# Kernel tuning notes

Hardware: AMD Instinct MI355X
Metric: run time of the kernel (lower is better)

Reference implementation:

```python
import jax, jax.numpy as jnp
import numpy as np


def setup_inputs() -> dict:
    key = jax.random.key(0)
    B, H, C, T = 8, 8, 64, 2048
    qkv = jax.random.normal(key, (B, 3 * H * C, T), dtype=jnp.float32)
    return {"qkv": qkv, "n_heads": H}


def reference(qkv, n_heads):
    # qkv: (B, 3*H*C, T)
    bs, width, length = qkv.shape
    ch = width // (3 * n_heads)
    q, k, v = jnp.split(qkv, 3, axis=1)          # each (B, H*C, T)
    scale = ch ** (-0.25)
    q = (q * scale).reshape(bs * n_heads, ch, length)
    k = (k * scale).reshape(bs * n_heads, ch, length)
    v = v.reshape(bs * n_heads, ch, length)
    # weight[b, t, s] = sum_c q[b,c,t] * k[b,c,s]
    weight = jnp.einsum('bct,bcs->bts', q, k)
    weight = jax.nn.softmax(weight.astype(jnp.float32), axis=-1).astype(qkv.dtype)
    out = jnp.einsum('bts,bcs->bct', weight, v)   # (B*H, C, T)
    return out.reshape(bs, n_heads * ch, length)
```

## Files before the change

### kernel.cpp

```cpp
#include <hip/hip_runtime.h>

typedef __bf16 bf16x4 __attribute__((ext_vector_type(4)));
typedef __bf16 bf16x8 __attribute__((ext_vector_type(8)));
typedef float floatx4 __attribute__((ext_vector_type(4)));
typedef float floatx16 __attribute__((ext_vector_type(16)));

#define T_SEQ 2048
#define TTILE 256
#define STILE 64
#define LOG2E_SCALE 0.18033688011112042f

__device__ __forceinline__ unsigned pack_bf16(float a, float b) {
    __bf16 x = (__bf16)a, y = (__bf16)b;
    unsigned short ux = __builtin_bit_cast(unsigned short, x);
    unsigned short uy = __builtin_bit_cast(unsigned short, y);
    return (unsigned)ux | ((unsigned)uy << 16);
}

__global__ __launch_bounds__(256, 2) void attn_fused(
    const float* __restrict__ qkv, float* __restrict__ out)
{
    __shared__ __align__(16) __bf16 Kt[STILE][72];
    __shared__ __align__(16) __bf16 Vs[64][72];

    const int tid  = threadIdx.x;
    const int lane = tid & 63;
    const int wave = tid >> 6;
    const int l31  = lane & 31;
    const int g    = lane >> 5;

    const int bh = blockIdx.y;
    const int b = bh >> 3, head = bh & 7;
    const size_t in_base = ((size_t)b * 1536 + head * 64) * T_SEQ;
    const float* Qg = qkv + in_base;
    const float* Kg = qkv + in_base + (size_t)512 * T_SEQ;
    const float* Vg = qkv + in_base + (size_t)1024 * T_SEQ;

    const int tcol0 = blockIdx.x * TTILE + wave * 64 + l31;
    const int tcol1 = tcol0 + 32;

    bf16x8 qf[2][4];
    #pragma unroll
    for (int kb = 0; kb < 4; ++kb)
        #pragma unroll
        for (int j = 0; j < 8; ++j) {
            size_t rowoff = (size_t)(kb * 16 + g * 8 + j) * T_SEQ;
            qf[0][kb][j] = (__bf16)Qg[rowoff + tcol0];
            qf[1][kb][j] = (__bf16)Qg[rowoff + tcol1];
        }

    floatx16 Oa[2][2];
    #pragma unroll
    for (int tt = 0; tt < 2; ++tt)
        #pragma unroll
        for (int mc = 0; mc < 2; ++mc)
            #pragma unroll
            for (int r = 0; r < 16; ++r) Oa[tt][mc][r] = 0.0f;
    float lsum0 = 0.0f, lsum1 = 0.0f;

    int cc[4], ss[4];
    size_t goff[4];
    #pragma unroll
    for (int r = 0; r < 4; ++r) {
        int i = tid + r * 256;
        cc[r] = i >> 4;
        ss[r] = (i & 15) * 4;
        goff[r] = (size_t)cc[r] * T_SEQ + ss[r];
    }
    const int ph = (tid >> 1) & 3;

    floatx4 kr[4], vr[4];
    #pragma unroll
    for (int r = 0; r < 4; ++r) {
        kr[r] = *(const floatx4*)(Kg + goff[r]);
        vr[r] = *(const floatx4*)(Vg + goff[r]);
    }

    for (int s0 = 0; s0 < T_SEQ; s0 += STILE) {
        __syncthreads();
        #pragma unroll
        for (int r = 0; r < 4; ++r) {
            int c = cc[r], s4 = ss[r];
            #pragma unroll
            for (int k = 0; k < 4; ++k) {
                int d = (k + ph) & 3;
                Kt[s4 + d][c] = (__bf16)kr[r][d];
            }
            bf16x4 vb;
            vb[0] = (__bf16)vr[r][0]; vb[1] = (__bf16)vr[r][1];
            vb[2] = (__bf16)vr[r][2]; vb[3] = (__bf16)vr[r][3];
            *(bf16x4*)&Vs[c][s4] = vb;
        }
        __syncthreads();

        if (s0 + STILE < T_SEQ) {
            #pragma unroll
            for (int r = 0; r < 4; ++r) {
                kr[r] = *(const floatx4*)(Kg + goff[r] + s0 + STILE);
                vr[r] = *(const floatx4*)(Vg + goff[r] + s0 + STILE);
            }
        }

        bf16x8 pf[2][4];
        #pragma unroll
        for (int ms = 0; ms < 2; ++ms) {
            floatx16 Sa0, Sa1;
            #pragma unroll
            for (int r = 0; r < 16; ++r) { Sa0[r] = 0.0f; Sa1[r] = 0.0f; }
            #pragma unroll
            for (int kb = 0; kb < 4; ++kb) {
                bf16x8 kf = *(const bf16x8*)&Kt[ms * 32 + l31][kb * 16 + g * 8];
                Sa0 = __builtin_amdgcn_mfma_f32_32x32x16_bf16(kf, qf[0][kb], Sa0, 0, 0, 0);
                Sa1 = __builtin_amdgcn_mfma_f32_32x32x16_bf16(kf, qf[1][kb], Sa1, 0, 0, 0);
            }
            #pragma unroll
            for (int tt = 0; tt < 2; ++tt) {
                const floatx16& Sa = tt ? Sa1 : Sa0;
                float p[16];
                #pragma unroll
                for (int r = 0; r < 16; ++r) {
                    p[r] = __builtin_amdgcn_exp2f(Sa[r] * LOG2E_SCALE);
                    if (tt) lsum1 += p[r]; else lsum0 += p[r];
                }
                unsigned d[8];
                #pragma unroll
                for (int q = 0; q < 8; ++q) d[q] = pack_bf16(p[2 * q], p[2 * q + 1]);
                #pragma unroll
                for (int kb = 0; kb < 2; ++kb) {
                    unsigned d0 = d[4 * kb + 0], d1 = d[4 * kb + 1];
                    unsigned d2 = d[4 * kb + 2], d3 = d[4 * kb + 3];
                    unsigned sendA = g ? d0 : d2;
                    unsigned sendB = g ? d1 : d3;
                    unsigned recvA = (unsigned)__shfl_xor((int)sendA, 32);
                    unsigned recvB = (unsigned)__shfl_xor((int)sendB, 32);
                    union { unsigned u[4]; bf16x8 v; } fu;
                    fu.u[0] = g ? recvA : d0;
                    fu.u[1] = g ? recvB : d1;
                    fu.u[2] = g ? d2    : recvA;
                    fu.u[3] = g ? d3    : recvB;
                    pf[tt][ms * 2 + kb] = fu.v;
                }
            }
        }

        #pragma unroll
        for (int mc = 0; mc < 2; ++mc)
            #pragma unroll
            for (int kb2 = 0; kb2 < 4; ++kb2) {
                bf16x8 vf = *(const bf16x8*)&Vs[mc * 32 + l31][kb2 * 16 + g * 8];
                Oa[0][mc] = __builtin_amdgcn_mfma_f32_32x32x16_bf16(vf, pf[0][kb2], Oa[0][mc], 0, 0, 0);
                Oa[1][mc] = __builtin_amdgcn_mfma_f32_32x32x16_bf16(vf, pf[1][kb2], Oa[1][mc], 0, 0, 0);
            }
    }

    float rl0 = 1.0f / (lsum0 + __shfl_xor(lsum0, 32));
    float rl1 = 1.0f / (lsum1 + __shfl_xor(lsum1, 32));

    const size_t out_base = ((size_t)b * 512 + head * 64) * T_SEQ;
    #pragma unroll
    for (int mc = 0; mc < 2; ++mc)
        #pragma unroll
        for (int r = 0; r < 16; ++r) {
            int c = mc * 32 + (r & 3) + 8 * (r >> 2) + 4 * g;
            size_t row = out_base + (size_t)c * T_SEQ;
            out[row + tcol0] = Oa[0][mc][r] * rl0;
            out[row + tcol1] = Oa[1][mc][r] * rl1;
        }
}

extern "C" void kernel_launch(void* const* d_in, const int* in_sizes, int n_in,
                              void* d_out, int out_size, void* d_ws, size_t ws_size,
                              hipStream_t stream) {
    const float* qkv = (const float*)d_in[0];
    float* out = (float*)d_out;
    dim3 grid(T_SEQ / TTILE, 64);
    attn_fused<<<grid, dim3(256), 0, stream>>>(qkv, out);
}
```

Before: 220.7 us.

## Widen T tile to 512 with 8 waves and compute row sums via MFMA

Doubles the query tile per block to 512 columns with 512 threads, so each staged K/V tile in shared memory is reused by eight waves instead of four and global K/V traffic is halved. The softmax scale is folded into Q at load time, which removes a multiply before every exp2. The per-lane VALU row-sum accumulation is replaced by extra MFMAs against a matrix of ones. The RNE bf16 conversions are swapped for add-and-truncate bit tricks. The trade-off is half as many blocks in the grid, which may leave CUs under-occupied, along with slightly different rounding behaviour.

New measurement: 210.3 us. 4.7% less time.

```diff
diff --git a/kernel.cpp b/kernel.cpp
--- a/kernel.cpp
+++ b/kernel.cpp
@@ -6,18 +6,20 @@
 typedef float floatx16 __attribute__((ext_vector_type(16)));
 
 #define T_SEQ 2048
-#define TTILE 256
+#define TTILE 512
 #define STILE 64
 #define LOG2E_SCALE 0.18033688011112042f
 
-__device__ __forceinline__ unsigned pack_bf16(float a, float b) {
-    __bf16 x = (__bf16)a, y = (__bf16)b;
-    unsigned short ux = __builtin_bit_cast(unsigned short, x);
-    unsigned short uy = __builtin_bit_cast(unsigned short, y);
-    return (unsigned)ux | ((unsigned)uy << 16);
+__device__ __forceinline__ unsigned pack_bf16_pair(float a, float b) {
+    unsigned ua = __builtin_bit_cast(unsigned, a) + 0x8000u;
+    unsigned ub = __builtin_bit_cast(unsigned, b) + 0x8000u;
+    return __builtin_amdgcn_perm(ub, ua, 0x07060302u);
+}
+__device__ __forceinline__ unsigned short bf16_bits(float a) {
+    return (unsigned short)((__builtin_bit_cast(unsigned, a) + 0x8000u) >> 16);
 }
 
-__global__ __launch_bounds__(256, 2) void attn_fused(
+__global__ __launch_bounds__(512, 2) void attn_fused(
     const float* __restrict__ qkv, float* __restrict__ out)
 {
     __shared__ __align__(16) __bf16 Kt[STILE][72];
@@ -45,33 +47,38 @@
         #pragma unroll
         for (int j = 0; j < 8; ++j) {
             size_t rowoff = (size_t)(kb * 16 + g * 8 + j) * T_SEQ;
-            qf[0][kb][j] = (__bf16)Qg[rowoff + tcol0];
-            qf[1][kb][j] = (__bf16)Qg[rowoff + tcol1];
+            qf[0][kb][j] = (__bf16)(Qg[rowoff + tcol0] * LOG2E_SCALE);
+            qf[1][kb][j] = (__bf16)(Qg[rowoff + tcol1] * LOG2E_SCALE);
         }
 
+    union { unsigned u[4]; bf16x8 v; } ones;
+    {
+        unsigned pat = (l31 == 0) ? 0x3F803F80u : 0u;
+        ones.u[0] = pat; ones.u[1] = pat; ones.u[2] = pat; ones.u[3] = pat;
+    }
+
     floatx16 Oa[2][2];
+    floatx16 La[2];
     #pragma unroll
-    for (int tt = 0; tt < 2; ++tt)
+    for (int tt = 0; tt < 2; ++tt) {
         #pragma unroll
-        for (int mc = 0; mc < 2; ++mc)
-            #pragma unroll
-            for (int r = 0; r < 16; ++r) Oa[tt][mc][r] = 0.0f;
-    float lsum0 = 0.0f, lsum1 = 0.0f;
+        for (int r = 0; r < 16; ++r) { Oa[tt][0][r] = 0.0f; Oa[tt][1][r] = 0.0f; La[tt][r] = 0.0f; }
+    }
 
-    int cc[4], ss[4];
-    size_t goff[4];
+    int cc[2], ss[2];
+    size_t goff[2];
     #pragma unroll
-    for (int r = 0; r < 4; ++r) {
-        int i = tid + r * 256;
+    for (int r = 0; r < 2; ++r) {
+        int i = tid + r * 512;
         cc[r] = i >> 4;
         ss[r] = (i & 15) * 4;
         goff[r] = (size_t)cc[r] * T_SEQ + ss[r];
     }
     const int ph = (tid >> 1) & 3;
 
-    floatx4 kr[4], vr[4];
+    floatx4 kr[2], vr[2];
     #pragma unroll
-    for (int r = 0; r < 4; ++r) {
+    for (int r = 0; r < 2; ++r) {
         kr[r] = *(const floatx4*)(Kg + goff[r]);
         vr[r] = *(const floatx4*)(Vg + goff[r]);
     }
@@ -79,23 +86,24 @@
     for (int s0 = 0; s0 < T_SEQ; s0 += STILE) {
         __syncthreads();
         #pragma unroll
-        for (int r = 0; r < 4; ++r) {
+        for (int r = 0; r < 2; ++r) {
             int c = cc[r], s4 = ss[r];
             #pragma unroll
             for (int k = 0; k < 4; ++k) {
                 int d = (k + ph) & 3;
-                Kt[s4 + d][c] = (__bf16)kr[r][d];
+                *(unsigned short*)&Kt[s4 + d][c] = bf16_bits(kr[r][d]);
             }
-            bf16x4 vb;
-            vb[0] = (__bf16)vr[r][0]; vb[1] = (__bf16)vr[r][1];
-            vb[2] = (__bf16)vr[r][2]; vb[3] = (__bf16)vr[r][3];
-            *(bf16x4*)&Vs[c][s4] = vb;
+            unsigned v01 = pack_bf16_pair(vr[r][0], vr[r][1]);
+            unsigned v23 = pack_bf16_pair(vr[r][2], vr[r][3]);
+            union { unsigned u[2]; bf16x4 v; } vb;
+            vb.u[0] = v01; vb.u[1] = v23;
+            *(bf16x4*)&Vs[c][s4] = vb.v;
         }
         __syncthreads();
 
         if (s0 + STILE < T_SEQ) {
             #pragma unroll
-            for (int r = 0; r < 4; ++r) {
+            for (int r = 0; r < 2; ++r) {
                 kr[r] = *(const floatx4*)(Kg + goff[r] + s0 + STILE);
                 vr[r] = *(const floatx4*)(Vg + goff[r] + s0 + STILE);
             }
@@ -118,13 +126,11 @@
                 const floatx16& Sa = tt ? Sa1 : Sa0;
                 float p[16];
                 #pragma unroll
-                for (int r = 0; r < 16; ++r) {
-                    p[r] = __builtin_amdgcn_exp2f(Sa[r] * LOG2E_SCALE);
-                    if (tt) lsum1 += p[r]; else lsum0 += p[r];
-                }
+                for (int r = 0; r < 16; ++r)
+                    p[r] = __builtin_amdgcn_exp2f(Sa[r]);
                 unsigned d[8];
                 #pragma unroll
-                for (int q = 0; q < 8; ++q) d[q] = pack_bf16(p[2 * q], p[2 * q + 1]);
+                for (int q = 0; q < 8; ++q) d[q] = pack_bf16_pair(p[2 * q], p[2 * q + 1]);
                 #pragma unroll
                 for (int kb = 0; kb < 2; ++kb) {
                     unsigned d0 = d[4 * kb + 0], d1 = d[4 * kb + 1];
@@ -151,10 +157,16 @@
                 Oa[0][mc] = __builtin_amdgcn_mfma_f32_32x32x16_bf16(vf, pf[0][kb2], Oa[0][mc], 0, 0, 0);
                 Oa[1][mc] = __builtin_amdgcn_mfma_f32_32x32x16_bf16(vf, pf[1][kb2], Oa[1][mc], 0, 0, 0);
             }
+        #pragma unroll
+        for (int kb2 = 0; kb2 < 4; ++kb2) {
+            La[0] = __builtin_amdgcn_mfma_f32_32x32x16_bf16(ones.v, pf[0][kb2], La[0], 0, 0, 0);
+            La[1] = __builtin_amdgcn_mfma_f32_32x32x16_bf16(ones.v, pf[1][kb2], La[1], 0, 0, 0);
+        }
     }
 
-    float rl0 = 1.0f / (lsum0 + __shfl_xor(lsum0, 32));
-    float rl1 = 1.0f / (lsum1 + __shfl_xor(lsum1, 32));
+    float d0 = La[0][0], d1 = La[1][0];
+    float rl0 = 1.0f / (d0 + __shfl_xor(d0, 32));
+    float rl1 = 1.0f / (d1 + __shfl_xor(d1, 32));
 
     const size_t out_base = ((size_t)b * 512 + head * 64) * T_SEQ;
     #pragma unroll
@@ -174,5 +186,5 @@
     const float* qkv = (const float*)d_in[0];
     float* out = (float*)d_out;
     dim3 grid(T_SEQ / TTILE, 64);
-    attn_fused<<<grid, dim3(256), 0, stream>>>(qkv, out);
+    attn_fused<<<grid, dim3(512), 0, stream>>>(qkv, out);
 }
```
